# Kernel tuning notes

Measured on AMD Instinct MI355X. Metric: run time of the kernel, lower is better.

Reference implementation:

```python
import jax, jax.numpy as jnp
import numpy as np

B, T, F = 32, 1024, 64
H = 128          # num_lstm_out
KH = 16          # kan_hidden_dim
C1, C2, C3 = 128, 256, 128
NC = 10


def _glorot(key, shape):
    fan_in = shape[0] if len(shape) == 2 else int(np.prod(shape[1:]))
    return (jax.random.normal(key, shape, jnp.float32) / np.sqrt(fan_in)).astype(jnp.float32)


def setup_inputs() -> dict:
    key = jax.random.key(0)
    ks = jax.random.split(key, 24)
    D = F + H
    d = {}
    d['x'] = jax.random.normal(ks[0], (B, T, F), jnp.float32)
    d['eps_z'] = jax.random.normal(ks[1], (B, H), jnp.float32)
    d['eps_cat'] = jax.random.normal(ks[2], (B, H), jnp.float32)
    # KAN-LSTM cell: gates = W2 @ silu(W1 @ [x;h])
    d['kan_w1'] = _glorot(ks[3], (D, KH)); d['kan_b1'] = jnp.zeros((KH,), jnp.float32)
    d['kan_w2'] = _glorot(ks[4], (KH, 4 * H)); d['kan_b2'] = jnp.zeros((4 * H,), jnp.float32)
    # causal convs (OIH layout)
    d['conv1_w'] = _glorot(ks[5], (C1, F, 8)); d['conv1_b'] = jnp.zeros((C1,), jnp.float32)
    d['conv2_w'] = _glorot(ks[6], (C2, C1, 5)); d['conv2_b'] = jnp.zeros((C2,), jnp.float32)
    d['conv3_w'] = _glorot(ks[7], (C3, C2, 3)); d['conv3_b'] = jnp.zeros((C3,), jnp.float32)
    # batchnorm affine params
    d['bn1_g'] = jnp.ones((C1,), jnp.float32); d['bn1_b'] = jnp.zeros((C1,), jnp.float32)
    d['bn2_g'] = jnp.ones((C2,), jnp.float32); d['bn2_b'] = jnp.zeros((C2,), jnp.float32)
    d['bn3_g'] = jnp.ones((C3,), jnp.float32); d['bn3_b'] = jnp.zeros((C3,), jnp.float32)
    # SE layers (reduction=16, no bias)
    d['se1_w1'] = _glorot(ks[8], (C1, C1 // 16)); d['se1_w2'] = _glorot(ks[9], (C1 // 16, C1))
    d['se2_w1'] = _glorot(ks[10], (C2, C2 // 16)); d['se2_w2'] = _glorot(ks[11], (C2 // 16, C2))
    # VIB heads
    d['fc_mu_w'] = _glorot(ks[12], (H, H)); d['fc_mu_b'] = jnp.zeros((H,), jnp.float32)
    d['fc_std_w'] = _glorot(ks[13], (H, H)); d['fc_std_b'] = jnp.zeros((H,), jnp.float32)
    d['fc_mu_cat_w'] = _glorot(ks[14], (2 * H, H)); d['fc_mu_cat_b'] = jnp.zeros((H,), jnp.float32)
    d['fc_std_cat_w'] = _glorot(ks[15], (2 * H, H)); d['fc_std_cat_b'] = jnp.zeros((H,), jnp.float32)
    d['fc_w'] = _glorot(ks[16], (H + C3, NC)); d['fc_b'] = jnp.zeros((NC,), jnp.float32)
    return d


def _kan_lstm(x, w1, b1, w2, b2):
    # x: (B,T,F) -> hidden (B,T,H); sequential recurrence via lax.scan
    xT = jnp.swapaxes(x, 0, 1)  # (T,B,F)
    h0 = jnp.zeros((x.shape[0], H), x.dtype)
    c0 = jnp.zeros((x.shape[0], H), x.dtype)

    def step(carry, xt):
        h, c = carry
        g = jax.nn.silu(jnp.concatenate([xt, h], axis=-1) @ w1 + b1) @ w2 + b2  # (B,4H)
        i_, f_, g_, o_ = jnp.split(g, 4, axis=-1)
        c = jax.nn.sigmoid(f_) * c + jax.nn.sigmoid(i_) * jnp.tanh(g_)
        h = jax.nn.sigmoid(o_) * jnp.tanh(c)
        return (h, c), h

    _, hs = jax.lax.scan(step, (h0, c0), xT)
    return jnp.swapaxes(hs, 0, 1)  # (B,T,H)


def _cluster_hidden(hidden):
    # hidden: (B,T,H). Pairwise cosine sim -> exp kernel -> best 2-block cut.
    Tn = hidden.shape[1]
    last = hidden[:, -1, :]
    hn = hidden / jnp.clip(jnp.linalg.norm(hidden, axis=-1, keepdims=True), 1e-8)
    S = jnp.exp(-5.5 * (1.0 - jnp.einsum('bik,bjk->bij', hn, hn)))  # (B,T,T)
    S = S * (1.0 - jnp.eye(Tn, dtype=S.dtype))  # zero diagonal
    # 2D prefix sums give all block sums in O(T^2) instead of O(T^3)
    P = jnp.cumsum(jnp.cumsum(S, axis=1), axis=2)
    i = jnp.arange(1, Tn)
    TL = P[:, i - 1, i - 1]                 # (B,T-1) sum of [:i,:i]
    full = P[:, -1, -1][:, None]
    TR = P[:, i - 1, -1] - TL               # sum of [:i,i:]
    BL = P[:, -1, i - 1] - TL               # sum of [i:,:i]
    BR = full - TL - TR - BL                # sum of [i:,i:]
    ii = i.astype(S.dtype)
    nn = (Tn - i).astype(S.dtype)
    dist = TL / (ii * ii) + BR / (nn * nn) - (TR + BL) / (ii * nn)
    cuts = jnp.argmax(dist, axis=1) + 1     # (B,)
    mask = (jnp.arange(Tn)[None, :] < cuts[:, None]).astype(hidden.dtype)
    corr = jnp.einsum('bt,bth->bh', mask, hidden) / cuts[:, None].astype(hidden.dtype)
    return last, corr


def _causal_conv(x, w, b):
    k = w.shape[-1]
    xp = jnp.pad(x, ((0, 0), (0, 0), (k - 1, 0)))
    y = jax.lax.conv_general_dilated(xp, w, (1,), 'VALID',
                                     dimension_numbers=('NCH', 'OIH', 'NCH'))
    return y + b[None, :, None]


def _bn(x, g, b, eps=1e-3):
    m = x.mean(axis=(0, 2), keepdims=True)
    v = x.var(axis=(0, 2), keepdims=True)
    return (x - m) / jnp.sqrt(v + eps) * g[None, :, None] + b[None, :, None]


def _se(x, w1, w2):
    y = x.mean(axis=2)                       # (B,C)
    y = jax.nn.sigmoid(jax.nn.relu(y @ w1) @ w2)
    return x * y[:, :, None]


def reference(x, eps_z, eps_cat, kan_w1, kan_b1, kan_w2, kan_b2,
              conv1_w, conv1_b, conv2_w, conv2_b, conv3_w, conv3_b,
              bn1_g, bn1_b, bn2_g, bn2_b, bn3_g, bn3_b,
              se1_w1, se1_w2, se2_w1, se2_w2,
              fc_mu_w, fc_mu_b, fc_std_w, fc_std_b,
              fc_mu_cat_w, fc_mu_cat_b, fc_std_cat_w, fc_std_cat_b,
              fc_w, fc_b):
    # LSTM branch
    hidden = _kan_lstm(x, kan_w1, kan_b1, kan_w2, kan_b2)      # (B,T,H)
    out, corr = _cluster_hidden(hidden)
    mu = corr @ fc_mu_w + fc_mu_b
    std = jax.nn.softplus(corr @ fc_std_w + fc_std_b)
    z = mu + std * eps_z
    xz = jnp.concatenate([out, z], axis=1)                      # (B,2H)
    mu_cat = xz @ fc_mu_cat_w + fc_mu_cat_b
    std_cat = jax.nn.softplus(xz @ fc_std_cat_w + fc_std_cat_b)
    x1 = mu_cat + std_cat * eps_cat   # dropout in eval mode = identity
    # FCN branch
    x2 = jnp.swapaxes(x, 1, 2)                                  # (B,F,T)
    x2 = jax.nn.gelu(_bn(_causal_conv(x2, conv1_w, conv1_b), bn1_g, bn1_b), approximate=False)
    x2 = _se(x2, se1_w1, se1_w2)
    x2 = jax.nn.gelu(_bn(_causal_conv(x2, conv2_w, conv2_b), bn2_g, bn2_b), approximate=False)
    x2 = _se(x2, se2_w1, se2_w2)
    x2 = jax.nn.gelu(_bn(_causal_conv(x2, conv3_w, conv3_b), bn3_g, bn3_b), approximate=False)
    x2 = x2.mean(axis=2)                                        # (B,C3)
    x_all = jnp.concatenate([x1, x2], axis=1)
    logits = x_all @ fc_w + fc_b
    return (jax.nn.log_softmax(logits, axis=1), mu, std, mu_cat, std_cat)
```

## Files before the change

kernel.cpp:

```cpp
#include <hip/hip_runtime.h>
#include <math.h>

#define B_ 32
#define T_ 1024
#define F_ 64
#define H_ 128
#define D_ 192
#define KH_ 16
#define C1_ 128
#define C2_ 256
#define C3_ 128
#define NC_ 10

typedef float v2f __attribute__((ext_vector_type(2)));
typedef float f32x4 __attribute__((ext_vector_type(4)));
typedef __bf16 bfrag __attribute__((ext_vector_type(8)));

__device__ __forceinline__ float sig_(float x){ return 1.f/(1.f+__expf(-x)); }
__device__ __forceinline__ float tanh_(float x){ return 1.f - 2.f/(__expf(2.f*x)+1.f); }
__device__ __forceinline__ float gelu_(float x){ return 0.5f*x*(1.f+erff(x*0.70710678118654752f)); }
__device__ __forceinline__ float softplus_(float x){ return fmaxf(x,0.f) + log1pf(__expf(-fabsf(x))); }

__device__ __forceinline__ unsigned bfpack(float a, float b){
  unsigned ua = __float_as_uint(a), ub = __float_as_uint(b);
  ua = ua + 0x7FFFu + ((ua>>16)&1u);
  ub = ub + 0x7FFFu + ((ub>>16)&1u);
  return (ua>>16) | (ub & 0xFFFF0000u);
}
__device__ __forceinline__ unsigned short bf1(float a){
  unsigned ua = __float_as_uint(a);
  ua = ua + 0x7FFFu + ((ua>>16)&1u);
  return (unsigned short)(ua>>16);
}
__device__ __forceinline__ float bf2f(unsigned short h){
  return __uint_as_float(((unsigned)h)<<16);
}

#define QPERM_XOR1(x) __int_as_float(__builtin_amdgcn_mov_dpp(__float_as_int(x), 0xB1, 0xF, 0xF, true))
#define QPERM_XOR2(x) __int_as_float(__builtin_amdgcn_mov_dpp(__float_as_int(x), 0x4E, 0xF, 0xF, true))

#define LDS_BARRIER() asm volatile("s_waitcnt lgkmcnt(0)\n\ts_barrier" ::: "memory")


__device__ __forceinline__ void ax_body(int blk, char* smemraw,
    const float* __restrict__ x, const float* __restrict__ w1, const float* __restrict__ b1,
    float* __restrict__ axT)
{
  struct AxS { float xs[16][68]; float w1s[64][16]; };
  AxS* sm = (AxS*)smemraw;
  const int bt0 = blk*16;
  const int tid = threadIdx.x;
  for(int i=tid;i<64*16;i+=256){ sm->w1s[i>>4][i&15] = w1[i]; }
  for(int i=tid;i<16*64;i+=256){ const int r=i>>6, d=i&63; sm->xs[r][d] = x[(size_t)(bt0+r)*64 + d]; }
  __syncthreads();
  const int r = tid>>4, j = tid&15;
  float s = b1[j];
  #pragma unroll
  for(int d=0; d<64; d++) s += sm->xs[r][d]*sm->w1s[d][j];
  const int bt = bt0 + r;
  axT[((size_t)(bt>>10)*16 + j)*1024 + (bt&1023)] = s;
}

__device__ __forceinline__ void prepack_body(int blk,
    const float* __restrict__ w1s, const float* __restrict__ w2s, const float* __restrict__ w3s,
    unsigned short* __restrict__ wp1, unsigned short* __restrict__ wp2, unsigned short* __restrict__ wp3)
{
  int e = blk*256 + threadIdx.x;
  if(e >= 65536+163840+98304) return;
  const float* w; unsigned short* wp; int Cout, Cin, Kw;
  if(e < 65536){ w=w1s; wp=wp1; Cout=C1_; Cin=F_;  Kw=8; }
  else if(e < 65536+163840){ e-=65536; w=w2s; wp=wp2; Cout=C2_; Cin=C1_; Kw=5; }
  else { e-=229376; w=w3s; wp=wp3; Cout=C3_; Cin=C2_; Kw=3; }
  const int co = e/(Cin*Kw);
  const int rem = e - co*(Cin*Kw);
  const int ci = rem/Kw, kw = rem - ci*Kw;
  const int off = (((ci>>5)*Kw + kw)*(Cout>>4) + (co>>4))*512 + ((co&15)*4 + ((ci>>3)&3))*8 + (ci&7);
  wp[off] = bf1(w[e]);
}

__device__ __forceinline__ void norm_body(int blk,
    const float* __restrict__ hidden,
    unsigned short* __restrict__ hnhi, unsigned short* __restrict__ hnlo)
{
  const int row = blk*8 + (threadIdx.x>>5);
  const int l = threadIdx.x&31;
  const float* hr = hidden + (size_t)row*H_;
  float s = 0.f;
  for(int k=l;k<H_;k+=32){ float v=hr[k]; s+=v*v; }
  #pragma unroll
  for(int m=16;m>=1;m>>=1) s += __shfl_xor(s, m, 64);
  const float inv = 1.f/fmaxf(sqrtf(s), 1e-8f);
  const float4 v = *(const float4*)&hr[l*4];
  const float f0=v.x*inv, f1=v.y*inv, f2=v.z*inv, f3=v.w*inv;
  const unsigned short h0=bf1(f0), h1=bf1(f1), h2=bf1(f2), h3=bf1(f3);
  uint2 phi; phi.x = (unsigned)h0 | ((unsigned)h1<<16); phi.y = (unsigned)h2 | ((unsigned)h3<<16);
  *(uint2*)&hnhi[(size_t)row*H_ + l*4] = phi;
  const unsigned short g0=bf1(f0-bf2f(h0)), g1=bf1(f1-bf2f(h1)), g2=bf1(f2-bf2f(h2)), g3=bf1(f3-bf2f(h3));
  uint2 plo; plo.x = (unsigned)g0 | ((unsigned)g1<<16); plo.y = (unsigned)g2 | ((unsigned)g3<<16);
  *(uint2*)&hnlo[(size_t)row*H_ + l*4] = plo;
}

struct SS {
  unsigned short Ahi[64*136];
  unsigned short Alo[64*136];
  unsigned short Bhi[64*136];
  unsigned short Blo[64*136];
  double red[64][17];
};
__device__ __forceinline__ void s_sym_body(int blk, char* smemraw,
    const unsigned short* __restrict__ hnhi, const unsigned short* __restrict__ hnlo,
    double* __restrict__ rowsum, double* __restrict__ psum)
{
  SS* sm = (SS*)smemraw;
  const int b = blk >> 4;
  const int k2 = blk & 15, k = k2 >> 1, half = k2 & 1;
  const int n1 = 16 - k;
  const int start = half ? 9 : 0;
  const int end   = half ? 17 : 9;
  const int tid = threadIdx.x, l = tid & 63, wv = tid >> 6;
  const int m = l & 15, q = l >> 4;
  const int arow = (wv*16 + m)*136;
  double* red = &sm->red[0][0];

  int cur_i0 = -1;
  for(int idx=start; idx<end; idx++){
    int i0, j0;
    if(idx < n1){ i0 = k*64;      j0 = (k+idx)*64; }
    else        { i0 = (15-k)*64; j0 = (15-k + (idx-n1))*64; }
    __syncthreads();
    if(i0 != cur_i0){
      cur_i0 = i0;
      const uint4* ghi = (const uint4*)(hnhi + ((size_t)b*T_ + i0)*H_);
      const uint4* glo = (const uint4*)(hnlo + ((size_t)b*T_ + i0)*H_);
      for(int t2=tid; t2<64*16; t2+=256){
        const int r = t2>>4, c8 = t2&15;
        *(uint4*)&sm->Ahi[r*136 + c8*8] = ghi[r*16 + c8];
        *(uint4*)&sm->Alo[r*136 + c8*8] = glo[r*16 + c8];
      }
    }
    {
      const uint4* ghi = (const uint4*)(hnhi + ((size_t)b*T_ + j0)*H_);
      const uint4* glo = (const uint4*)(hnlo + ((size_t)b*T_ + j0)*H_);
      for(int t2=tid; t2<64*16; t2+=256){
        const int r = t2>>4, c8 = t2&15;
        *(uint4*)&sm->Bhi[r*136 + c8*8] = ghi[r*16 + c8];
        *(uint4*)&sm->Blo[r*136 + c8*8] = glo[r*16 + c8];
      }
    }
    __syncthreads();

    f32x4 acc[4];
    #pragma unroll
    for(int nt=0;nt<4;nt++) acc[nt] = (f32x4)(0.f);
    #pragma unroll
    for(int kc=0;kc<4;kc++){
      const bfrag Ah = *(const bfrag*)&sm->Ahi[arow + kc*32 + q*8];
      const bfrag Al = *(const bfrag*)&sm->Alo[arow + kc*32 + q*8];
      #pragma unroll
      for(int nt=0;nt<4;nt++){
        const int brow = (nt*16 + m)*136 + kc*32 + q*8;
        const bfrag Bh = *(const bfrag*)&sm->Bhi[brow];
        const bfrag Bl = *(const bfrag*)&sm->Blo[brow];
        acc[nt] = __builtin_amdgcn_mfma_f32_16x16x32_bf16(Ah, Bh, acc[nt], 0, 0, 0);
        acc[nt] = __builtin_amdgcn_mfma_f32_16x16x32_bf16(Al, Bh, acc[nt], 0, 0, 0);
        acc[nt] = __builtin_amdgcn_mfma_f32_16x16x32_bf16(Ah, Bl, acc[nt], 0, 0, 0);
      }
    }

    if(i0 == j0){
      double rs[4]={0,0,0,0}, ps[4]={0,0,0,0};
      #pragma unroll
      for(int nt=0;nt<4;nt++){
        const int gj = j0 + nt*16 + m;
        #pragma unroll
        for(int r=0;r<4;r++){
          const int gi = i0 + wv*16 + q*4 + r;
          if(gi == gj) continue;
          const float sv = __expf(-5.5f*(1.f - acc[nt][r]));
          rs[r] += (double)sv;
          if(gj < gi) ps[r] += (double)sv;
        }
      }
      #pragma unroll
      for(int r=0;r<4;r++){
        #pragma unroll
        for(int mk=1;mk<16;mk<<=1){
          rs[r] += __shfl_xor(rs[r], mk, 64);
          ps[r] += __shfl_xor(ps[r], mk, 64);
        }
      }
      if(m == 0){
        const size_t gbase = (size_t)b*T_ + i0 + wv*16 + q*4;
        #pragma unroll
        for(int r=0;r<4;r++){
          unsafeAtomicAdd(&rowsum[gbase + r], rs[r]);
          unsafeAtomicAdd(&psum[gbase + r], ps[r]);
        }
      }
    } else {
      double rs[4]={0,0,0,0}, cs[4]={0,0,0,0};
      #pragma unroll
      for(int nt=0;nt<4;nt++){
        double csn = 0.0;
        #pragma unroll
        for(int r=0;r<4;r++){
          const float sv = __expf(-5.5f*(1.f - acc[nt][r]));
          rs[r] += (double)sv;
          csn   += (double)sv;
        }
        cs[nt] = csn;
      }
      #pragma unroll
      for(int r=0;r<4;r++){
        #pragma unroll
        for(int mk=1;mk<16;mk<<=1) rs[r] += __shfl_xor(rs[r], mk, 64);
      }
      if(m == 0){
        const size_t gbase = (size_t)b*T_ + i0 + wv*16 + q*4;
        #pragma unroll
        for(int r=0;r<4;r++) unsafeAtomicAdd(&rowsum[gbase + r], rs[r]);
      }
      #pragma unroll
      for(int nt=0;nt<4;nt++){
        cs[nt] += __shfl_xor(cs[nt], 16, 64);
        cs[nt] += __shfl_xor(cs[nt], 32, 64);
      }
      if(q == 0){
        #pragma unroll
        for(int nt=0;nt<4;nt++) red[wv*64 + nt*16 + m] = cs[nt];
      }
      __syncthreads();
      if(tid < 64){
        const double v = red[tid] + red[64+tid] + red[128+tid] + red[192+tid];
        unsafeAtomicAdd(&rowsum[(size_t)b*T_ + j0 + tid], v);
        unsafeAtomicAdd(&psum[(size_t)b*T_ + j0 + tid], v);
      }
    }
  }
}

struct CS {
  double sr[256]; double sp[256]; double bd[256]; double totR;
  float c2[2][128]; int bidx[256]; int cut;
};
__device__ __forceinline__ void cluster_body(int b, char* smemraw,
    const double* __restrict__ rowsum, const double* __restrict__ psum,
    const float* __restrict__ hidden, float* __restrict__ corr, int* __restrict__ cuts)
{
  CS* sm = (CS*)smemraw;
  const int tid = threadIdx.x;
  const double* r = rowsum + (size_t)b*T_;
  const double* p = psum + (size_t)b*T_;
  double r4[4], p4[4];
  #pragma unroll
  for(int q=0;q<4;q++){ r4[q]=r[tid*4+q]; p4[q]=p[tid*4+q]; }
  sm->sr[tid]=r4[0]+r4[1]+r4[2]+r4[3];
  sm->sp[tid]=p4[0]+p4[1]+p4[2]+p4[3];
  __syncthreads();
  if(tid==0){
    double ar=0, ap=0;
    for(int i=0;i<256;i++){ double tr=sm->sr[i], tp=sm->sp[i]; sm->sr[i]=ar; sm->sp[i]=ap; ar+=tr; ap+=tp; }
    sm->totR = ar;
  }
  __syncthreads();
  double cr = sm->sr[tid], cp = sm->sp[tid];
  const double full = sm->totR;
  double best = -1e308; int bi = 1;
  #pragma unroll
  for(int q=0;q<4;q++){
    cr += r4[q]; cp += p4[q];
    const int i = 4*tid + q + 1;
    if(i < T_){
      const double TL = 2.0*cp;
      const double TRv = cr - TL;
      const double BR = full - TL - 2.0*TRv;
      const double di = (double)i, dn = (double)(T_-i);
      const double dist = TL/(di*di) + BR/(dn*dn) - (2.0*TRv)/(di*dn);
      if(dist > best){ best=dist; bi=i; }
    }
  }
  sm->bd[tid]=best; sm->bidx[tid]=bi;
  __syncthreads();
  if(tid==0){
    double bb=-1e308; int ii=1;
    for(int q=0;q<256;q++){ if(sm->bd[q]>bb){ bb=sm->bd[q]; ii=sm->bidx[q]; } }
    sm->cut=ii; cuts[b]=ii;
  }
  __syncthreads();
  const int cut = sm->cut;
  const int h = tid&127, half = tid>>7;
  float s=0.f;
  const float* hb = hidden + (size_t)b*T_*H_;
  #pragma unroll 4
  for(int t=half; t<cut; t+=2) s += hb[(size_t)t*H_ + h];
  sm->c2[half][h]=s;
  __syncthreads();
  if(tid<128) corr[b*H_+tid] = (sm->c2[0][tid]+sm->c2[1][tid])/(float)cut;
}

__device__ __forceinline__ void head1_body(int b, char* smemraw,
    const float* __restrict__ corr, const float* __restrict__ hidden,
    const float* __restrict__ eps_z, const float* __restrict__ eps_cat,
    const float* __restrict__ mu_w, const float* __restrict__ mu_b,
    const float* __restrict__ std_w, const float* __restrict__ std_b,
    const float* __restrict__ muc_w, const float* __restrict__ muc_b,
    const float* __restrict__ stdc_w, const float* __restrict__ stdc_b,
    float* __restrict__ out_mu, float* __restrict__ out_std,
    float* __restrict__ out_muc, float* __restrict__ out_stdc, float* __restrict__ x1)
{
  struct H1 { float cs[128]; float xz[256]; };
  H1* sm = (H1*)smemraw;
  const int h = threadIdx.x;
  if(h<128){
    sm->cs[h]=corr[b*H_+h];
    sm->xz[h]=hidden[((size_t)b*T_ + (T_-1))*H_ + h];
  }
  __syncthreads();
  if(h<128){
    float m=mu_b[h], sdv=std_b[h];
    for(int k=0;k<H_;k++){ const float cv=sm->cs[k]; m+=cv*mu_w[k*H_+h]; sdv+=cv*std_w[k*H_+h]; }
    const float stdv = softplus_(sdv);
    out_mu[b*H_+h]=m; out_std[b*H_+h]=stdv;
    sm->xz[128+h] = m + stdv*eps_z[b*H_+h];
  }
  __syncthreads();
  if(h<128){
    float mc=muc_b[h], sc=stdc_b[h];
    for(int k=0;k<256;k++){ const float v=sm->xz[k]; mc+=v*muc_w[k*H_+h]; sc+=v*stdc_w[k*H_+h]; }
    const float stdc = softplus_(sc);
    out_muc[b*H_+h]=mc; out_stdc[b*H_+h]=stdc;
    x1[b*H_+h]=mc + stdc*eps_cat[b*H_+h];
  }
}

struct ConvS {
  float sescale[256];
  float seh[16];
  unsigned short xs[72*40];
};
__device__ __forceinline__ void conv_body(int bx, int by, int bz, char* smemraw,
    const float* __restrict__ in, const unsigned short* __restrict__ wp,
    const float* __restrict__ bias,
    const float* __restrict__ se_in, const float* __restrict__ se_w1,
    const float* __restrict__ se_w2, int seR,
    float* __restrict__ y, float* __restrict__ bnacc, int Cin, int Cout, int Kw)
{
  ConvS* sm = (ConvS*)smemraw;
  unsigned short* xs = sm->xs;
  const int b = bz, t0 = bx*64, co0 = by*64;
  const int tid = threadIdx.x, l = tid&63, wv = tid>>6;
  const int q = l>>4, m = l&15;
  const int TW = 64 + Kw - 1;
  const int abase = (wv*16 + m)*40 + q*8;
  const int boff = (m*4 + q)*8;
  const bool use_se = (se_in != nullptr);

  if(use_se){
    float* ms = (float*)xs;
    if(tid<Cin) ms[tid] = se_in[b*Cin+tid] * (1.f/(float)T_);
    __syncthreads();
    if(tid<seR){ float s=0.f; for(int k=0;k<Cin;k++) s += ms[k]*se_w1[k*seR+tid]; sm->seh[tid]=fmaxf(s,0.f); }
    __syncthreads();
    if(tid<Cin){ float s=0.f; for(int k=0;k<seR;k++) s += sm->seh[k]*se_w2[k*Cin+tid]; sm->sescale[tid]=sig_(s); }
  }

  f32x4 acc[4];
  #pragma unroll
  for(int nt=0;nt<4;nt++) acc[nt] = (f32x4)(0.f);

  const int nchunks = Cin >> 5;
  for(int cc=0; cc<nchunks; cc++){
    __syncthreads();
    for(int idx=tid; idx<TW*8; idx+=256){
      const int r = idx>>3, c4 = (idx&7)*4;
      const int tg = t0 - (Kw-1) + r;
      uint2 pk = make_uint2(0u, 0u);
      if(tg >= 0){
        float4 v = *(const float4*)&in[((size_t)b*T_ + tg)*Cin + cc*32 + c4];
        if(use_se){
          const float4 s4 = *(const float4*)&sm->sescale[cc*32 + c4];
          v.x*=s4.x; v.y*=s4.y; v.z*=s4.z; v.w*=s4.w;
        }
        pk.x = bfpack(v.x, v.y); pk.y = bfpack(v.z, v.w);
      }
      *(uint2*)&xs[r*40 + c4] = pk;
    }
    __syncthreads();
    for(int kw=0; kw<Kw; kw++){
      const bfrag Af = *(const bfrag*)&xs[abase + kw*40];
      #pragma unroll
      for(int nt=0; nt<4; nt++){
        const unsigned short* wpp = wp + ((size_t)((cc*Kw + kw)*(Cout>>4) + (by*4 + nt)))*512 + boff;
        const bfrag Bf = *(const bfrag*)wpp;
        acc[nt] = __builtin_amdgcn_mfma_f32_16x16x32_bf16(Af, Bf, acc[nt], 0, 0, 0);
      }
    }
  }
  __syncthreads();
  float* part = (float*)xs;
  const int t_base = t0 + wv*16 + q*4;
  #pragma unroll
  for(int nt=0; nt<4; nt++){
    const int co = co0 + nt*16 + m;
    const float bv = bias[co];
    float s1 = 0.f, s2 = 0.f;
    #pragma unroll
    for(int r=0;r<4;r++){
      const float v = acc[nt][r] + bv;
      y[((size_t)b*T_ + t_base + r)*Cout + co] = v;
      s1 += v; s2 += v*v;
    }
    s1 += __shfl_xor(s1, 16); s1 += __shfl_xor(s1, 32);
    s2 += __shfl_xor(s2, 16); s2 += __shfl_xor(s2, 32);
    if(q==0){ part[(wv*64 + nt*16 + m)*2+0] = s1; part[(wv*64 + nt*16 + m)*2+1] = s2; }
  }
  __syncthreads();
  if(tid < 64){
    float a1=0.f, a2=0.f;
    #pragma unroll
    for(int w2i=0; w2i<4; w2i++){ a1 += part[(w2i*64+tid)*2+0]; a2 += part[(w2i*64+tid)*2+1]; }
    atomicAdd(&bnacc[co0 + tid], a1);
    atomicAdd(&bnacc[Cout + co0 + tid], a2);
  }
}

__device__ __forceinline__ void bn_act_body(int b, int chunk, char* smemraw,
    float* __restrict__ y, const float* __restrict__ bnacc,
    const float* __restrict__ gw, const float* __restrict__ bw,
    float* __restrict__ mean_acc, int C, int write_y)
{
  const int t0 = chunk*128, tid = threadIdx.x;
  const int c = tid & (C-1), part = tid / C, np = 256 / C;
  const float cnt = (float)(B_*T_);
  const float mm = bnacc[c]/cnt;
  const float var = bnacc[C+c]/cnt - mm*mm;
  const float sc = gw[c]/sqrtf(var+1e-3f);
  const float sh = bw[c] - mm*sc;
  float s = 0.f;
  for(int t=t0+part; t<t0+128; t+=np){
    const size_t off = ((size_t)b*T_ + t)*C + c;
    float v = y[off];
    v = gelu_(v*sc + sh);
    if(write_y) y[off] = v;
    s += v;
  }
  float* rs = (float*)smemraw;
  if(np > 1){
    rs[tid]=s;
    __syncthreads();
    if(part==0) s += rs[tid+C];
  }
  if(part==0) atomicAdd(&mean_acc[b*C+c], s);
}

__device__ __forceinline__ void lstm_seg_body(int b, int ts, int nsteps, char* smemraw,
    const float* __restrict__ axT, const float* __restrict__ w1,
    const float* __restrict__ w2, const float* __restrict__ b2,
    float* __restrict__ hidden, float* __restrict__ cstate)
{
  float (*hs)[148] = (float(*)[148])smemraw;
  const int tid = threadIdx.x;
  const int l = tid & 63, wv = tid >> 6;
  const int j = l >> 2, g = l & 3;
  const int hi = wv*64 + l;

  v2f w1hv[16];
  #pragma unroll
  for(int q=0;q<16;q++){
    w1hv[q].x = w1[(64 + g*32 + 2*q)*KH_ + j];
    w1hv[q].y = w1[(64 + g*32 + 2*q + 1)*KH_ + j];
  }
  v2f w2if[16], w2go[16];
  #pragma unroll
  for(int k=0;k<16;k++){
    w2if[k].x = w2[k*512 + hi];       w2if[k].y = w2[k*512 + 128 + hi];
    w2go[k].x = w2[k*512 + 256 + hi]; w2go[k].y = w2[k*512 + 384 + hi];
  }
  v2f bif, bgo;
  bif.x = b2[hi]; bif.y = b2[128+hi]; bgo.x = b2[256+hi]; bgo.y = b2[384+hi];

  const float* axr = axT + ((size_t)b*16 + j)*1024;
  float* hb = hidden + (size_t)b*T_*H_;
  const int hwi = (hi>>5)*36 + (hi&31);
  float c;
  if(ts == 0){
    for(int i=tid;i<2*148;i+=128) ((float*)hs)[i]=0.f;
    c = 0.f;
  } else {
    c = cstate[b*H_ + hi];
    hs[0][hwi] = hb[(size_t)(ts-1)*H_ + hi];
  }
  float4 axA = *(const float4*)&axr[ts];
  float4 axB = *(const float4*)&axr[ts+4];
  __syncthreads();

#define LSTM_STEP(tt, axv, RB) { \
    const float* hsr = hs[RB]; \
    float* hsw = hs[1-(RB)]; \
    v2f ap0=(v2f)(0.f), ap1=(v2f)(0.f), ap2=(v2f)(0.f), ap3=(v2f)(0.f); \
    { const float4 hv = *(const float4*)&hsr[g*36 + 0];  ap0 += ((v2f){hv.x,hv.y})*w1hv[0]  + ((v2f){hv.z,hv.w})*w1hv[1]; } \
    { const float4 hv = *(const float4*)&hsr[g*36 + 4];  ap1 += ((v2f){hv.x,hv.y})*w1hv[2]  + ((v2f){hv.z,hv.w})*w1hv[3]; } \
    { const float4 hv = *(const float4*)&hsr[g*36 + 8];  ap2 += ((v2f){hv.x,hv.y})*w1hv[4]  + ((v2f){hv.z,hv.w})*w1hv[5]; } \
    { const float4 hv = *(const float4*)&hsr[g*36 + 12]; ap3 += ((v2f){hv.x,hv.y})*w1hv[6]  + ((v2f){hv.z,hv.w})*w1hv[7]; } \
    { const float4 hv = *(const float4*)&hsr[g*36 + 16]; ap0 += ((v2f){hv.x,hv.y})*w1hv[8]  + ((v2f){hv.z,hv.w})*w1hv[9]; } \
    { const float4 hv = *(const float4*)&hsr[g*36 + 20]; ap1 += ((v2f){hv.x,hv.y})*w1hv[10] + ((v2f){hv.z,hv.w})*w1hv[11]; } \
    { const float4 hv = *(const float4*)&hsr[g*36 + 24]; ap2 += ((v2f){hv.x,hv.y})*w1hv[12] + ((v2f){hv.z,hv.w})*w1hv[13]; } \
    { const float4 hv = *(const float4*)&hsr[g*36 + 28]; ap3 += ((v2f){hv.x,hv.y})*w1hv[14] + ((v2f){hv.z,hv.w})*w1hv[15]; } \
    const v2f apt = (ap0+ap1)+(ap2+ap3); \
    float a = apt.x + apt.y; \
    a += QPERM_XOR1(a); \
    a += QPERM_XOR2(a); \
    a += (axv); \
    const float g1 = a * sig_(a); \
    v2f aIF = bif, aGO = bgo; \
    _Pragma("unroll") \
    for(int k=0;k<16;k++){ \
      const float gk = __int_as_float(__builtin_amdgcn_readlane(__float_as_int(g1), 4*k)); \
      v2f gk2; gk2.x=gk; gk2.y=gk; \
      aIF += gk2 * w2if[k]; \
      aGO += gk2 * w2go[k]; \
    } \
    const float si = sig_(aIF.x); \
    const float sf = sig_(aIF.y); \
    const float tg = tanh_(aGO.x); \
    const float so = sig_(aGO.y); \
    c = sf*c + si*tg; \
    const float h = so * tanh_(c); \
    hsw[hwi] = h; \
    hb[(size_t)(tt)*H_ + hi] = h; \
    LDS_BARRIER(); \
  }

  const int te = ts + nsteps;
  for(int t0=ts;t0<te;t0+=4){
    const int tl = (t0+8 < 1020) ? (t0+8) : 1020;
    const float4 axC = *(const float4*)&axr[tl];
    LSTM_STEP(t0+0, axA.x, 0)
    LSTM_STEP(t0+1, axA.y, 1)
    LSTM_STEP(t0+2, axA.z, 0)
    LSTM_STEP(t0+3, axA.w, 1)
    axA = axB; axB = axC;
  }
#undef LSTM_STEP
  if(te < T_) cstate[b*H_ + hi] = c;
}


__global__ __launch_bounds__(256) void mega0_kernel(
    const float* c1w, const float* c2w, const float* c3w,
    unsigned short* wp1, unsigned short* wp2, unsigned short* wp3,
    const float* x, const float* kw1, const float* kb1, float* axT)
{
  __shared__ __align__(16) char sm[16*68*4 + 64*16*4];
  const int bid = blockIdx.x;
  if(bid < 1280) prepack_body(bid, c1w, c2w, c3w, wp1, wp2, wp3);
  else ax_body(bid-1280, sm, x, kw1, kb1, axT);
}

__global__ __launch_bounds__(256) void seg_kernel(
    int ts, int nsteps, int phase,
    const float* axT, const float* kw1, const float* kw2, const float* kb2,
    float* hidden, float* cstate,
    const float* x, const unsigned short* wp1, const float* c1b, float* y1, float* bn1,
    const float* g1w, const float* b1w, float* se1_in,
    const unsigned short* wp2, const float* c2b, const float* s1w1, const float* s1w2,
    float* y2, float* bn2,
    const float* g2w, const float* b2w, float* se2_in,
    const unsigned short* wp3, const float* c3b, const float* s2w1, const float* s2w2,
    float* y3, float* bn3,
    const float* g3w, const float* b3w, float* x2)
{
  __shared__ __align__(16) char sm[sizeof(ConvS)];
  const int bid = blockIdx.x;
  if(bid < 32){
    if(threadIdx.x >= 128){
      const int nb = nsteps + 1;
      #pragma nounroll
      for(int i=0;i<nb;i++){ asm volatile("s_barrier" ::: "memory"); }
      return;
    }
    __builtin_amdgcn_s_setprio(1);
    lstm_seg_body(bid, ts, nsteps, sm, axT, kw1, kw2, kb2, hidden, cstate);
    return;
  }
  const int cb = bid - 32;
  switch(phase){
    case 0:
      conv_body(cb&15, (cb>>4)&1, cb>>5, sm, x, wp1, c1b,
                nullptr, nullptr, nullptr, 0, y1, bn1, F_, C1_, 8);
      break;
    case 1:
      bn_act_body(cb>>3, cb&7, sm, y1, bn1, g1w, b1w, se1_in, C1_, 1);
      break;
    case 2:
      conv_body(cb&15, (cb>>4)&3, cb>>6, sm, y1, wp2, c2b,
                se1_in, s1w1, s1w2, C1_/16, y2, bn2, C1_, C2_, 5);
      break;
    case 3:
      bn_act_body(cb>>3, cb&7, sm, y2, bn2, g2w, b2w, se2_in, C2_, 1);
      break;
    case 4:
      conv_body(cb&15, (cb>>4)&1, cb>>5, sm, y2, wp3, c3b,
                se2_in, s2w1, s2w2, C2_/16, y3, bn3, C2_, C3_, 3);
      break;
    default:
      bn_act_body(cb>>3, cb&7, sm, y3, bn3, g3w, b3w, x2, C3_, 0);
      break;
  }
}

__global__ __launch_bounds__(256) void norm_kernel(
    const float* hidden, unsigned short* hnhi, unsigned short* hnlo)
{
  norm_body(blockIdx.x, hidden, hnhi, hnlo);
}

__global__ __launch_bounds__(256) void s_kernel(
    const unsigned short* hnhi, const unsigned short* hnlo, double* rowsum, double* psum)
{
  __shared__ __align__(16) char sm[sizeof(SS)];
  s_sym_body(blockIdx.x, sm, hnhi, hnlo, rowsum, psum);
}

__global__ __launch_bounds__(256) void tail_kernel(
    const double* rowsum, const double* psum, const float* hidden, float* corr, int* cuts,
    const float* eps_z, const float* eps_cat,
    const float* mu_w, const float* mu_b, const float* std_w, const float* std_b,
    const float* muc_w, const float* muc_b, const float* stdc_w, const float* stdc_b,
    float* out_mu, float* out_std, float* out_muc, float* out_stdc, float* x1,
    const float* x2, const float* fcw, const float* fcb, float* outls)
{
  __shared__ __align__(16) char sm[sizeof(CS)];
  const int b = blockIdx.x, tid = threadIdx.x;
  cluster_body(b, sm, rowsum, psum, hidden, corr, cuts);
  __syncthreads();
  head1_body(b, sm, corr, hidden, eps_z, eps_cat, mu_w, mu_b, std_w, std_b,
             muc_w, muc_b, stdc_w, stdc_b, out_mu, out_std, out_muc, out_stdc, x1);
  __syncthreads();
  struct H2 { float xa[256]; float lg[NC_]; };
  H2* s2 = (H2*)sm;
  s2->xa[tid] = (tid<128) ? x1[b*128+tid] : x2[b*128+(tid-128)]*(1.f/(float)T_);
  __syncthreads();
  if(tid<NC_){
    float s = fcb[tid];
    for(int k=0;k<256;k++) s += s2->xa[k]*fcw[k*NC_+tid];
    s2->lg[tid]=s;
  }
  __syncthreads();
  if(tid==0){
    float mx=s2->lg[0];
    for(int q=1;q<NC_;q++) mx=fmaxf(mx,s2->lg[q]);
    float se=0;
    for(int q=0;q<NC_;q++) se += __expf(s2->lg[q]-mx);
    const float lse = logf(se)+mx;
    for(int q=0;q<NC_;q++) outls[b*NC_+q] = s2->lg[q]-lse;
  }
}

extern "C" void kernel_launch(void* const* d_in, const int* in_sizes, int n_in,
                              void* d_out, int out_size, void* d_ws, size_t ws_size,
                              hipStream_t stream) {
  (void)in_sizes; (void)n_in; (void)out_size; (void)ws_size;
  const float* x        = (const float*)d_in[0];
  const float* eps_z    = (const float*)d_in[1];
  const float* eps_cat  = (const float*)d_in[2];
  const float* kan_w1   = (const float*)d_in[3];
  const float* kan_b1   = (const float*)d_in[4];
  const float* kan_w2   = (const float*)d_in[5];
  const float* kan_b2   = (const float*)d_in[6];
  const float* conv1_w  = (const float*)d_in[7];
  const float* conv1_b  = (const float*)d_in[8];
  const float* conv2_w  = (const float*)d_in[9];
  const float* conv2_b  = (const float*)d_in[10];
  const float* conv3_w  = (const float*)d_in[11];
  const float* conv3_b  = (const float*)d_in[12];
  const float* bn1_g    = (const float*)d_in[13];
  const float* bn1_b    = (const float*)d_in[14];
  const float* bn2_g    = (const float*)d_in[15];
  const float* bn2_b    = (const float*)d_in[16];
  const float* bn3_g    = (const float*)d_in[17];
  const float* bn3_b    = (const float*)d_in[18];
  const float* se1_w1   = (const float*)d_in[19];
  const float* se1_w2   = (const float*)d_in[20];
  const float* se2_w1   = (const float*)d_in[21];
  const float* se2_w2   = (const float*)d_in[22];
  const float* fc_mu_w  = (const float*)d_in[23];
  const float* fc_mu_b  = (const float*)d_in[24];
  const float* fc_std_w = (const float*)d_in[25];
  const float* fc_std_b = (const float*)d_in[26];
  const float* fc_muc_w = (const float*)d_in[27];
  const float* fc_muc_b = (const float*)d_in[28];
  const float* fc_stdc_w= (const float*)d_in[29];
  const float* fc_stdc_b= (const float*)d_in[30];
  const float* fc_w     = (const float*)d_in[31];
  const float* fc_b     = (const float*)d_in[32];

  float* out = (float*)d_out;
  float* out_ls   = out;
  float* out_mu   = out + 320;
  float* out_std  = out + 320 + 4096;
  float* out_muc  = out + 320 + 2*4096;
  float* out_stdc = out + 320 + 3*4096;

  float* ws = (float*)d_ws;
  const size_t SZ_HID = (size_t)B_*T_*H_;
  const size_t SZ_Y1  = (size_t)B_*T_*C1_;
  const size_t SZ_Y2  = (size_t)B_*T_*C2_;
  float*  hidden = ws;
  float*  y1     = hidden + SZ_HID;
  float*  y2     = y1 + SZ_Y1;
  double* rowsum = (double*)(y2 + SZ_Y2);
  double* psum   = rowsum + (size_t)B_*T_;
  float*  corr   = (float*)(psum + (size_t)B_*T_);
  float*  x1     = corr + (size_t)B_*H_;
  float*  bnbuf  = x1 + (size_t)B_*H_;
  float*  bn1    = bnbuf;
  float*  bn2    = bnbuf + 2*C1_;
  float*  bn3    = bnbuf + 2*C1_ + 2*C2_;
  float*  se1_in = bnbuf + 1024;
  float*  se2_in = se1_in + (size_t)B_*C1_;
  float*  x2     = se2_in + (size_t)B_*C2_;
  int*    cuts   = (int*)(x2 + (size_t)B_*C3_);
  float*  cstate = (float*)(cuts + B_);
  float*  axbuf  = cstate + (size_t)B_*H_;
  unsigned short* wp1 = (unsigned short*)(axbuf + (size_t)B_*16*T_);
  unsigned short* wp2 = wp1 + (size_t)C1_*F_*8;
  unsigned short* wp3 = wp2 + (size_t)C2_*C1_*5;
  unsigned short* hnhi = wp3 + (size_t)C3_*C2_*3;
  unsigned short* hnlo = hnhi + (size_t)B_*T_*H_;
  float*  y3     = y1;

  hipMemsetAsync(bnbuf, 0, (size_t)(1024 + B_*C1_ + B_*C2_ + B_*C3_)*sizeof(float), stream);
  hipMemsetAsync(rowsum, 0, (size_t)2*B_*T_*sizeof(double), stream);

  mega0_kernel<<<3328, 256, 0, stream>>>(conv1_w, conv2_w, conv3_w, wp1, wp2, wp3,
                                         x, kan_w1, kan_b1, axbuf);

  #define SEG_ARGS axbuf, kan_w1, kan_w2, kan_b2, hidden, cstate, \
      x, wp1, conv1_b, y1, bn1, bn1_g, bn1_b, se1_in, \
      wp2, conv2_b, se1_w1, se1_w2, y2, bn2, bn2_g, bn2_b, se2_in, \
      wp3, conv3_b, se2_w1, se2_w2, y3, bn3, bn3_g, bn3_b, x2
  seg_kernel<<<32 + 1024, 256, 0, stream>>>(  0, 144, 0, SEG_ARGS);
  seg_kernel<<<32 +  256, 256, 0, stream>>>(144,  64, 1, SEG_ARGS);
  seg_kernel<<<32 + 2048, 256, 0, stream>>>(208, 384, 2, SEG_ARGS);
  seg_kernel<<<32 +  256, 256, 0, stream>>>(592,  64, 3, SEG_ARGS);
  seg_kernel<<<32 + 1024, 256, 0, stream>>>(656, 240, 4, SEG_ARGS);
  seg_kernel<<<32 +  256, 256, 0, stream>>>(896, 128, 5, SEG_ARGS);
  #undef SEG_ARGS

  norm_kernel<<<4096, 256, 0, stream>>>(hidden, hnhi, hnlo);
  s_kernel<<<512, 256, 0, stream>>>(hnhi, hnlo, rowsum, psum);
  tail_kernel<<<B_, 256, 0, stream>>>(rowsum, psum, hidden, corr, cuts,
      eps_z, eps_cat,
      fc_mu_w, fc_mu_b, fc_std_w, fc_std_b, fc_muc_w, fc_muc_b, fc_stdc_w, fc_stdc_b,
      out_mu, out_std, out_muc, out_stdc, x1,
      x2, fc_w, fc_b, out_ls);
}
```

Before: 773.4 us.

## Overlap norm, chunk sums and similarity tiles with LSTM recurrence segments

Moves the hidden-state normalisation, per-64-step chunk sums and the triangular similarity tile work out of separate post-LSTM kernels. They now run as extra blocks inside the LSTM segment kernels, processing hidden rows already produced by earlier segments. Part of the weight prepacking also moves into the first segment launch. The cluster mean uses the precomputed chunk sums plus a short tail loop instead of summing all rows. This hides serial tail work behind the latency-bound recurrence, at the cost of complex scheduling parameters, contention with the LSTM blocks, and a new similarity tile ordering.

```diff
diff --git a/kernel.cpp b/kernel.cpp
--- a/kernel.cpp
+++ b/kernel.cpp
@@ -78,13 +78,13 @@
   wp[off] = bf1(w[e]);
 }
 
-__device__ __forceinline__ void norm_body(int blk,
+__device__ __forceinline__ void norm8_body(size_t rowbase,
     const float* __restrict__ hidden,
     unsigned short* __restrict__ hnhi, unsigned short* __restrict__ hnlo)
 {
-  const int row = blk*8 + (threadIdx.x>>5);
+  const size_t row = rowbase + (threadIdx.x>>5);
   const int l = threadIdx.x&31;
-  const float* hr = hidden + (size_t)row*H_;
+  const float* hr = hidden + row*H_;
   float s = 0.f;
   for(int k=l;k<H_;k+=32){ float v=hr[k]; s+=v*v; }
   #pragma unroll
@@ -94,10 +94,23 @@
   const float f0=v.x*inv, f1=v.y*inv, f2=v.z*inv, f3=v.w*inv;
   const unsigned short h0=bf1(f0), h1=bf1(f1), h2=bf1(f2), h3=bf1(f3);
   uint2 phi; phi.x = (unsigned)h0 | ((unsigned)h1<<16); phi.y = (unsigned)h2 | ((unsigned)h3<<16);
-  *(uint2*)&hnhi[(size_t)row*H_ + l*4] = phi;
+  *(uint2*)&hnhi[row*H_ + l*4] = phi;
   const unsigned short g0=bf1(f0-bf2f(h0)), g1=bf1(f1-bf2f(h1)), g2=bf1(f2-bf2f(h2)), g3=bf1(f3-bf2f(h3));
   uint2 plo; plo.x = (unsigned)g0 | ((unsigned)g1<<16); plo.y = (unsigned)g2 | ((unsigned)g3<<16);
-  *(uint2*)&hnlo[(size_t)row*H_ + l*4] = plo;
+  *(uint2*)&hnlo[row*H_ + l*4] = plo;
+}
+
+__device__ __forceinline__ void chunk_body(int b, int c, char* smemraw,
+    const float* __restrict__ hidden, float* __restrict__ chunksum)
+{
+  float* red = (float*)smemraw;
+  const int tid = threadIdx.x, h = tid&127, half = tid>>7;
+  const float* hb = hidden + ((size_t)b*T_ + c*64)*H_;
+  float s = 0.f;
+  for(int t=half; t<64; t+=2) s += hb[(size_t)t*H_ + h];
+  if(half==1) red[h] = s;
+  __syncthreads();
+  if(half==0) chunksum[((size_t)b*16 + c)*H_ + h] = s + red[h];
 }
 
 struct SS {
@@ -107,44 +120,42 @@
   unsigned short Blo[64*136];
   double red[64][17];
 };
-__device__ __forceinline__ void s_sym_body(int blk, char* smemraw,
+__device__ __forceinline__ void s_list_body(int b, int f0, int cnt, char* smemraw,
     const unsigned short* __restrict__ hnhi, const unsigned short* __restrict__ hnlo,
     double* __restrict__ rowsum, double* __restrict__ psum)
 {
   SS* sm = (SS*)smemraw;
-  const int b = blk >> 4;
-  const int k2 = blk & 15, k = k2 >> 1, half = k2 & 1;
-  const int n1 = 16 - k;
-  const int start = half ? 9 : 0;
-  const int end   = half ? 17 : 9;
   const int tid = threadIdx.x, l = tid & 63, wv = tid >> 6;
   const int m = l & 15, q = l >> 4;
   const int arow = (wv*16 + m)*136;
   double* red = &sm->red[0][0];
-
-  int cur_i0 = -1;
-  for(int idx=start; idx<end; idx++){
-    int i0, j0;
-    if(idx < n1){ i0 = k*64;      j0 = (k+idx)*64; }
-    else        { i0 = (15-k)*64; j0 = (15-k + (idx-n1))*64; }
+  int curj = -1;
+
+  for(int f=f0; f<f0+cnt; f++){
+    int j = (int)((sqrtf(8.f*(float)f + 1.f) - 1.f)*0.5f);
+    while((j*(j+1))/2 > f) j--;
+    while(((j+1)*(j+2))/2 <= f) j++;
+    const int i = f - (j*(j+1))/2;
+    const int i0 = i*64, j0 = j*64;
+
     __syncthreads();
-    if(i0 != cur_i0){
-      cur_i0 = i0;
+    if(j != curj){
+      curj = j;
+      const uint4* ghi = (const uint4*)(hnhi + ((size_t)b*T_ + j0)*H_);
+      const uint4* glo = (const uint4*)(hnlo + ((size_t)b*T_ + j0)*H_);
+      for(int t2=tid; t2<64*16; t2+=256){
+        const int r = t2>>4, c8 = t2&15;
+        *(uint4*)&sm->Bhi[r*136 + c8*8] = ghi[r*16 + c8];
+        *(uint4*)&sm->Blo[r*136 + c8*8] = glo[r*16 + c8];
+      }
+    }
+    {
       const uint4* ghi = (const uint4*)(hnhi + ((size_t)b*T_ + i0)*H_);
       const uint4* glo = (const uint4*)(hnlo + ((size_t)b*T_ + i0)*H_);
       for(int t2=tid; t2<64*16; t2+=256){
         const int r = t2>>4, c8 = t2&15;
         *(uint4*)&sm->Ahi[r*136 + c8*8] = ghi[r*16 + c8];
         *(uint4*)&sm->Alo[r*136 + c8*8] = glo[r*16 + c8];
-      }
-    }
-    {
-      const uint4* ghi = (const uint4*)(hnhi + ((size_t)b*T_ + j0)*H_);
-      const uint4* glo = (const uint4*)(hnlo + ((size_t)b*T_ + j0)*H_);
-      for(int t2=tid; t2<64*16; t2+=256){
-        const int r = t2>>4, c8 = t2&15;
-        *(uint4*)&sm->Bhi[r*136 + c8*8] = ghi[r*16 + c8];
-        *(uint4*)&sm->Blo[r*136 + c8*8] = glo[r*16 + c8];
       }
     }
     __syncthreads();
@@ -245,7 +256,8 @@
 };
 __device__ __forceinline__ void cluster_body(int b, char* smemraw,
     const double* __restrict__ rowsum, const double* __restrict__ psum,
-    const float* __restrict__ hidden, float* __restrict__ corr, int* __restrict__ cuts)
+    const float* __restrict__ hidden, const float* __restrict__ chunksum,
+    float* __restrict__ corr, int* __restrict__ cuts)
 {
   CS* sm = (CS*)smemraw;
   const int tid = threadIdx.x;
@@ -290,9 +302,13 @@
   const int cut = sm->cut;
   const int h = tid&127, half = tid>>7;
   float s=0.f;
-  const float* hb = hidden + (size_t)b*T_*H_;
-  #pragma unroll 4
-  for(int t=half; t<cut; t+=2) s += hb[(size_t)t*H_ + h];
+  if(half==0){
+    const int cf = cut>>6;
+    for(int c=0;c<cf;c++) s += chunksum[((size_t)b*16 + c)*H_ + h];
+  } else {
+    const float* hb = hidden + (size_t)b*T_*H_;
+    for(int t=(cut & ~63); t<cut; t++) s += hb[(size_t)t*H_ + h];
+  }
   sm->c2[half][h]=s;
   __syncthreads();
   if(tid<128) corr[b*H_+tid] = (sm->c2[0][tid]+sm->c2[1][tid])/(float)cut;
@@ -553,12 +569,13 @@
 {
   __shared__ __align__(16) char sm[16*68*4 + 64*16*4];
   const int bid = blockIdx.x;
-  if(bid < 1280) prepack_body(bid, c1w, c2w, c3w, wp1, wp2, wp3);
-  else ax_body(bid-1280, sm, x, kw1, kb1, axT);
+  if(bid < 256) prepack_body(bid, c1w, c2w, c3w, wp1, wp2, wp3);
+  else ax_body(bid-256, sm, x, kw1, kb1, axT);
 }
 
 __global__ __launch_bounds__(256) void seg_kernel(
-    int ts, int nsteps, int phase,
+    int ts, int nsteps, int phase, int nphase, int nxtra,
+    int nr0, int nnorm, int c0, int nchunk,
     const float* axT, const float* kw1, const float* kw2, const float* kb2,
     float* hidden, float* cstate,
     const float* x, const unsigned short* wp1, const float* c1b, float* y1, float* bn1,
@@ -568,11 +585,14 @@
     const float* g2w, const float* b2w, float* se2_in,
     const unsigned short* wp3, const float* c3b, const float* s2w1, const float* s2w2,
     float* y3, float* bn3,
-    const float* g3w, const float* b3w, float* x2)
+    const float* c1w, const float* c2w, const float* c3w,
+    unsigned short* wp1o, unsigned short* wp2o, unsigned short* wp3o,
+    unsigned short* hnhi, unsigned short* hnlo, float* chunksum)
 {
   __shared__ __align__(16) char sm[sizeof(ConvS)];
   const int bid = blockIdx.x;
   if(bid < 32){
+    if(nsteps == 0) return;
     if(threadIdx.x >= 128){
       const int nb = nsteps + 1;
       #pragma nounroll
@@ -583,47 +603,104 @@
     lstm_seg_body(bid, ts, nsteps, sm, axT, kw1, kw2, kb2, hidden, cstate);
     return;
   }
-  const int cb = bid - 32;
-  switch(phase){
-    case 0:
-      conv_body(cb&15, (cb>>4)&1, cb>>5, sm, x, wp1, c1b,
-                nullptr, nullptr, nullptr, 0, y1, bn1, F_, C1_, 8);
-      break;
-    case 1:
-      bn_act_body(cb>>3, cb&7, sm, y1, bn1, g1w, b1w, se1_in, C1_, 1);
-      break;
-    case 2:
-      conv_body(cb&15, (cb>>4)&3, cb>>6, sm, y1, wp2, c2b,
-                se1_in, s1w1, s1w2, C1_/16, y2, bn2, C1_, C2_, 5);
-      break;
-    case 3:
-      bn_act_body(cb>>3, cb&7, sm, y2, bn2, g2w, b2w, se2_in, C2_, 1);
-      break;
-    case 4:
-      conv_body(cb&15, (cb>>4)&1, cb>>5, sm, y2, wp3, c3b,
-                se2_in, s2w1, s2w2, C2_/16, y3, bn3, C2_, C3_, 3);
-      break;
-    default:
-      bn_act_body(cb>>3, cb&7, sm, y3, bn3, g3w, b3w, x2, C3_, 0);
-      break;
-  }
-}
-
-__global__ __launch_bounds__(256) void norm_kernel(
-    const float* hidden, unsigned short* hnhi, unsigned short* hnlo)
-{
-  norm_body(blockIdx.x, hidden, hnhi, hnlo);
-}
-
-__global__ __launch_bounds__(256) void s_kernel(
-    const unsigned short* hnhi, const unsigned short* hnlo, double* rowsum, double* psum)
+  int cb = bid - 32;
+  if(cb < nphase){
+    switch(phase){
+      case 0:
+        conv_body(cb&15, (cb>>4)&1, cb>>5, sm, x, wp1, c1b,
+                  nullptr, nullptr, nullptr, 0, y1, bn1, F_, C1_, 8);
+        break;
+      case 1:
+        bn_act_body(cb>>3, cb&7, sm, y1, bn1, g1w, b1w, se1_in, C1_, 1);
+        break;
+      case 2:
+        conv_body(cb&15, (cb>>4)&3, cb>>6, sm, y1, wp2, c2b,
+                  se1_in, s1w1, s1w2, C1_/16, y2, bn2, C1_, C2_, 5);
+        break;
+      case 3:
+        bn_act_body(cb>>3, cb&7, sm, y2, bn2, g2w, b2w, se2_in, C2_, 1);
+        break;
+      default:
+        conv_body(cb&15, (cb>>4)&1, cb>>5, sm, y2, wp3, c3b,
+                  se2_in, s2w1, s2w2, C2_/16, y3, bn3, C2_, C3_, 3);
+        break;
+    }
+    return;
+  }
+  cb -= nphase;
+  if(cb < nxtra){ prepack_body(256 + cb, c1w, c2w, c3w, wp1o, wp2o, wp3o); return; }
+  cb -= nxtra;
+  if(cb < nnorm){
+    const int b = cb & 31, tb = cb >> 5;
+    norm8_body((size_t)b*T_ + nr0 + tb*8, hidden, hnhi, hnlo);
+    return;
+  }
+  cb -= nnorm;
+  if(cb < nchunk){
+    const int b = cb & 31;
+    chunk_body(b, c0 + (cb>>5), sm, hidden, chunksum);
+  }
+}
+
+__global__ __launch_bounds__(256) void segS_kernel(
+    int ts, int nsteps, int nbn3,
+    int nr0, int nnorm, int c0, int nchunk,
+    int smode, int sringlo, int nstile,
+    const float* axT, const float* kw1, const float* kw2, const float* kb2,
+    float* hidden, float* cstate,
+    float* y3, const float* bn3, const float* g3w, const float* b3w, float* x2,
+    unsigned short* hnhi, unsigned short* hnlo, float* chunksum,
+    double* rowsum, double* psum)
 {
   __shared__ __align__(16) char sm[sizeof(SS)];
-  s_sym_body(blockIdx.x, sm, hnhi, hnlo, rowsum, psum);
+  const int bid = blockIdx.x;
+  if(bid < 32){
+    if(nsteps == 0) return;
+    if(threadIdx.x >= 128){
+      const int nb = nsteps + 1;
+      #pragma nounroll
+      for(int i=0;i<nb;i++){ asm volatile("s_barrier" ::: "memory"); }
+      return;
+    }
+    __builtin_amdgcn_s_setprio(1);
+    lstm_seg_body(bid, ts, nsteps, sm, axT, kw1, kw2, kb2, hidden, cstate);
+    return;
+  }
+  int cb = bid - 32;
+  if(cb < nbn3){
+    bn_act_body(cb>>3, cb&7, sm, y3, bn3, g3w, b3w, x2, C3_, 0);
+    return;
+  }
+  cb -= nbn3;
+  if(cb < nnorm){
+    const int b = cb & 31, tb = cb >> 5;
+    norm8_body((size_t)b*T_ + nr0 + tb*8, hidden, hnhi, hnlo);
+    return;
+  }
+  cb -= nnorm;
+  if(cb < nchunk){
+    const int b = cb & 31;
+    chunk_body(b, c0 + (cb>>5), sm, hidden, chunksum);
+    return;
+  }
+  cb -= nchunk;
+  if(cb < nstile){
+    const int b = cb & 31, k = cb >> 5;
+    int f0, cnt;
+    if(smode == 1){
+      const int m = sringlo + k;
+      f0 = (m*(m+1))/2; cnt = m + 1;
+    } else {
+      f0 = 55 + ((k<9) ? 7*k : 63 + 6*(k-9));
+      cnt = (k<9) ? 7 : 6;
+    }
+    s_list_body(b, f0, cnt, sm, hnhi, hnlo, rowsum, psum);
+  }
 }
 
 __global__ __launch_bounds__(256) void tail_kernel(
-    const double* rowsum, const double* psum, const float* hidden, float* corr, int* cuts,
+    const double* rowsum, const double* psum, const float* hidden,
+    const float* chunksum, float* corr, int* cuts,
     const float* eps_z, const float* eps_cat,
     const float* mu_w, const float* mu_b, const float* std_w, const float* std_b,
     const float* muc_w, const float* muc_b, const float* stdc_w, const float* stdc_b,
@@ -632,7 +709,7 @@
 {
   __shared__ __align__(16) char sm[sizeof(CS)];
   const int b = blockIdx.x, tid = threadIdx.x;
-  cluster_body(b, sm, rowsum, psum, hidden, corr, cuts);
+  cluster_body(b, sm, rowsum, psum, hidden, chunksum, corr, cuts);
   __syncthreads();
   head1_body(b, sm, corr, hidden, eps_z, eps_cat, mu_w, mu_b, std_w, std_b,
              muc_w, muc_b, stdc_w, stdc_b, out_mu, out_std, out_muc, out_stdc, x1);
@@ -722,7 +799,8 @@
   float*  x2     = se2_in + (size_t)B_*C2_;
   int*    cuts   = (int*)(x2 + (size_t)B_*C3_);
   float*  cstate = (float*)(cuts + B_);
-  float*  axbuf  = cstate + (size_t)B_*H_;
+  float*  chunksum = cstate + (size_t)B_*H_;
+  float*  axbuf  = chunksum + (size_t)B_*16*H_;
   unsigned short* wp1 = (unsigned short*)(axbuf + (size_t)B_*16*T_);
   unsigned short* wp2 = wp1 + (size_t)C1_*F_*8;
   unsigned short* wp3 = wp2 + (size_t)C2_*C1_*5;
@@ -733,24 +811,41 @@
   hipMemsetAsync(bnbuf, 0, (size_t)(1024 + B_*C1_ + B_*C2_ + B_*C3_)*sizeof(float), stream);
   hipMemsetAsync(rowsum, 0, (size_t)2*B_*T_*sizeof(double), stream);
 
-  mega0_kernel<<<3328, 256, 0, stream>>>(conv1_w, conv2_w, conv3_w, wp1, wp2, wp3,
+  mega0_kernel<<<2304, 256, 0, stream>>>(conv1_w, conv2_w, conv3_w, wp1, wp2, wp3,
                                          x, kan_w1, kan_b1, axbuf);
 
   #define SEG_ARGS axbuf, kan_w1, kan_w2, kan_b2, hidden, cstate, \
       x, wp1, conv1_b, y1, bn1, bn1_g, bn1_b, se1_in, \
       wp2, conv2_b, se1_w1, se1_w2, y2, bn2, bn2_g, bn2_b, se2_in, \
-      wp3, conv3_b, se2_w1, se2_w2, y3, bn3, bn3_g, bn3_b, x2
-  seg_kernel<<<32 + 1024, 256, 0, stream>>>(  0, 144, 0, SEG_ARGS);
-  seg_kernel<<<32 +  256, 256, 0, stream>>>(144,  64, 1, SEG_ARGS);
-  seg_kernel<<<32 + 2048, 256, 0, stream>>>(208, 384, 2, SEG_ARGS);
-  seg_kernel<<<32 +  256, 256, 0, stream>>>(592,  64, 3, SEG_ARGS);
-  seg_kernel<<<32 + 1024, 256, 0, stream>>>(656, 240, 4, SEG_ARGS);
-  seg_kernel<<<32 +  256, 256, 0, stream>>>(896, 128, 5, SEG_ARGS);
+      wp3, conv3_b, se2_w1, se2_w2, y3, bn3, \
+      conv1_w, conv2_w, conv3_w, wp1, wp2, wp3, \
+      hnhi, hnlo, chunksum
+  seg_kernel<<<32+1024+1024, 256, 0, stream>>>(  0,144, 0,1024,1024,   0,   0,  0,  0, SEG_ARGS);
+  seg_kernel<<<32+256+576,   256, 0, stream>>>(144, 64, 1, 256,   0,   0, 576,  0,  0, SEG_ARGS);
+  seg_kernel<<<32+2048+256+96,256,0, stream>>>(208,384, 2,2048,   0, 144, 256,  0, 96, SEG_ARGS);
+  seg_kernel<<<32+256+1536+192,256,0,stream>>>(592, 64, 3, 256,   0, 208,1536,  3,192, SEG_ARGS);
+  seg_kernel<<<32+1024+256+32,256,0, stream>>>(656,240, 4,1024,   0, 592, 256,  9, 32, SEG_ARGS);
   #undef SEG_ARGS
 
-  norm_kernel<<<4096, 256, 0, stream>>>(hidden, hnhi, hnlo);
-  s_kernel<<<512, 256, 0, stream>>>(hnhi, hnlo, rowsum, psum);
-  tail_kernel<<<B_, 256, 0, stream>>>(rowsum, psum, hidden, corr, cuts,
+  #define SEGS_ARGS axbuf, kan_w1, kan_w2, kan_b2, hidden, cstate, \
+      y3, bn3, bn3_g, bn3_b, x2, hnhi, hnlo, chunksum, rowsum, psum
+  segS_kernel<<<32+256+960+128+320, 256, 0, stream>>>(
+      896, 128, 256, 656, 960, 10, 128, 1, 0, 320, SEGS_ARGS);
+  {
+    #define SEG_ARGS axbuf, kan_w1, kan_w2, kan_b2, hidden, cstate, \
+        x, wp1, conv1_b, y1, bn1, bn1_g, bn1_b, se1_in, \
+        wp2, conv2_b, se1_w1, se1_w2, y2, bn2, bn2_g, bn2_b, se2_in, \
+        wp3, conv3_b, se2_w1, se2_w2, y3, bn3, \
+        conv1_w, conv2_w, conv3_w, wp1, wp2, wp3, \
+        hnhi, hnlo, chunksum
+    seg_kernel<<<32+512+64, 256, 0, stream>>>(0, 0, -1, 0, 0, 896, 512, 14, 64, SEG_ARGS);
+    #undef SEG_ARGS
+  }
+  segS_kernel<<<32+384, 256, 0, stream>>>(
+      0, 0, 0, 0, 0, 0, 0, 2, 0, 384, SEGS_ARGS);
+  #undef SEGS_ARGS
+
+  tail_kernel<<<B_, 256, 0, stream>>>(rowsum, psum, hidden, chunksum, corr, cuts,
       eps_z, eps_cat,
       fc_mu_w, fc_mu_b, fc_std_w, fc_std_b, fc_muc_w, fc_muc_b, fc_stdc_w, fc_stdc_b,
       out_mu, out_std, out_muc, out_stdc, x1,
```

Measured after the change: 726.1 us. -6.1%, faster.
